# Performance work log

Hardware: AMD Instinct MI355X
Metric: run time of the kernel (lower is better)

The kernel has to match this reference:

```python
import jax, jax.numpy as jnp
import numpy as np

E = 1024   # d_model
H = 16     # nhead
DH = E // H
F = 4096   # dim_feedforward
B, S = 4, 1024
EPS = 1e-5


def setup_inputs() -> dict:
    key = jax.random.key(0)
    ks = jax.random.split(key, 12)
    s = 0.02
    return {
        "src": jax.random.normal(ks[0], (B, S, E), jnp.float32),
        "src_mask": jnp.zeros((S, S), jnp.float32),
        "w_qkv": jax.random.normal(ks[1], (3 * E, E), jnp.float32) * s,
        "b_qkv": jnp.zeros((3 * E,), jnp.float32),
        "w_o": jax.random.normal(ks[2], (E, E), jnp.float32) * s,
        "b_o": jnp.zeros((E,), jnp.float32),
        "w1": jax.random.normal(ks[3], (F, E), jnp.float32) * s,
        "b1": jnp.zeros((F,), jnp.float32),
        "w2": jax.random.normal(ks[4], (E, F), jnp.float32) * s,
        "b2": jnp.zeros((E,), jnp.float32),
        "ln1_g": jnp.ones((E,), jnp.float32),
        "ln1_b": jnp.zeros((E,), jnp.float32),
        "ln2_g": jnp.ones((E,), jnp.float32),
        "ln2_b": jnp.zeros((E,), jnp.float32),
    }


def _layer_norm(x, g, b):
    mu = jnp.mean(x, axis=-1, keepdims=True)
    var = jnp.mean(jnp.square(x - mu), axis=-1, keepdims=True)
    return (x - mu) * jax.lax.rsqrt(var + EPS) * g + b


def reference(src, src_mask, w_qkv, b_qkv, w_o, b_o, w1, b1, w2, b2,
              ln1_g, ln1_b, ln2_g, ln2_b):
    # dropout in eval mode (identity). Math matches nn.MultiheadAttention
    # with need_weights=True, average_attn_weights=False.
    b, s, e = src.shape
    qkv = src @ w_qkv.T + b_qkv                      # [B,S,3E]
    q, k, v = jnp.split(qkv, 3, axis=-1)
    q = q.reshape(b, s, H, DH)
    k = k.reshape(b, s, H, DH)
    v = v.reshape(b, s, H, DH)
    scale = 1.0 / np.sqrt(DH)
    scores = jnp.einsum('bqhd,bkhd->bhqk', q, k) * scale + src_mask  # [B,H,S,S]
    attn_weights = jax.nn.softmax(scores, axis=-1)                   # [B,H,S,S]
    ctx = jnp.einsum('bhqk,bkhd->bqhd', attn_weights, v).reshape(b, s, e)
    attn_out = ctx @ w_o.T + b_o
    x = _layer_norm(src + attn_out, ln1_g, ln1_b)
    ffn = jax.nn.relu(x @ w1.T + b1) @ w2.T + b2
    x = _layer_norm(x + ffn, ln2_g, ln2_b)
    return x, attn_weights
```

## Files before the change

kernel.cpp:

```cpp
#include <hip/hip_runtime.h>
#include <cstdint>

typedef __bf16 bf16;
typedef bf16 bf16x8 __attribute__((ext_vector_type(8)));
typedef bf16 bf16x4 __attribute__((ext_vector_type(4)));
typedef float f32x4 __attribute__((ext_vector_type(4)));
typedef uint32_t u32;

static constexpr int E_ = 1024;
static constexpr int H_ = 16;
static constexpr int DH_ = 64;
static constexpr int F_ = 4096;
static constexpr int B_ = 4;
static constexpr int S_ = 1024;
static constexpr long TOK = (long)B_ * S_;

__device__ static __forceinline__ void gld16(const void* g, void* l) {
  __builtin_amdgcn_global_load_lds(
      (const __attribute__((address_space(1))) u32*)g,
      (__attribute__((address_space(3))) u32*)l, 16, 0, 0);
}

__device__ __forceinline__ f32x4 mfma16(bf16x8 a, bf16x8 b, f32x4 c) {
  return __builtin_amdgcn_mfma_f32_16x16x32_bf16(a, b, c, 0, 0, 0);
}

__global__ __launch_bounds__(256) void f2b_all(
    const float* __restrict__ s0, bf16* __restrict__ d0,
    const float* __restrict__ s1, bf16* __restrict__ d1,
    const float* __restrict__ s2, bf16* __restrict__ d2,
    const float* __restrict__ s3, bf16* __restrict__ d3,
    const float* __restrict__ s4, bf16* __restrict__ d4) {
  long v = (long)blockIdx.x * 256 + threadIdx.x;
  const float* in;
  bf16* out;
  long off;
  if (v < 524288)        { in = s0; out = d0; off = v; }
  else if (v < 917504)   { in = s1; out = d1; off = v - 524288; }
  else if (v < 1048576)  { in = s2; out = d2; off = v - 917504; }
  else if (v < 1572864)  { in = s3; out = d3; off = v - 1048576; }
  else                   { in = s4; out = d4; off = v - 1572864; }
  const float4* p = (const float4*)in + off * 2;
  float4 a = p[0], b = p[1];
  bf16x8 o = {(bf16)a.x, (bf16)a.y, (bf16)a.z, (bf16)a.w,
              (bf16)b.x, (bf16)b.y, (bf16)b.z, (bf16)b.w};
  *((bf16x8*)out + off) = o;
}

enum { G_RELU_BF16 = 0, G_QKV = 1 };

template <int EPI>
__global__ __launch_bounds__(512, 2) void gemm256(
    const bf16* __restrict__ A, const bf16* __restrict__ Bm,
    bf16* __restrict__ Cb, bf16* __restrict__ Qh, bf16* __restrict__ Kh,
    bf16* __restrict__ Vt, const float* __restrict__ bias, int K, int ldc) {
  __shared__ bf16 S[65536];
  bf16* A0 = S;
  bf16* A1 = S + 16384;
  bf16* B0 = S + 32768;
  bf16* B1 = S + 49152;
  const int tid = threadIdx.x, lane = tid & 63, wave = tid >> 6;
  const int quad = lane >> 4, l16 = lane & 15;
  const int wm = wave >> 2, wn = wave & 3;
  const int row0 = blockIdx.y * 256, col0 = blockIdx.x * 256;
  const int NT = K >> 6;

  const long ldab = (long)K * 2;
  const char* Ag = (const char*)A + (long)(row0 + (tid >> 3)) * ldab + (tid & 7) * 16;
  const char* Bg = (const char*)Bm + (long)(col0 + (tid >> 3)) * ldab + (tid & 7) * 16;
  char* A0c = (char*)A0 + tid * 16;
  char* A1c = (char*)A1 + tid * 16;
  char* B0c = (char*)B0 + tid * 16;
  char* B1c = (char*)B1 + tid * 16;

  f32x4 acc[8][4];
#pragma unroll
  for (int m = 0; m < 8; m++)
#pragma unroll
    for (int n = 0; n < 4; n++) acc[m][n] = (f32x4){0.f, 0.f, 0.f, 0.f};

#pragma unroll
  for (int c = 0; c < 4; c++) gld16(Ag + (long)c * 64 * ldab, A0c + c * 8192);
#pragma unroll
  for (int c = 0; c < 4; c++) gld16(Bg + (long)c * 64 * ldab, B0c + c * 8192);
#pragma unroll
  for (int c = 0; c < 4; c++) gld16(Ag + (long)c * 64 * ldab + 128, A1c + c * 8192);

  auto tile = [&](int kt, const bf16* Ac, const bf16* Bc, char* AcS, char* BoS,
                  bool last) {
    if (last)
      asm volatile("s_waitcnt vmcnt(0)" ::: "memory");
    else
      asm volatile("s_waitcnt vmcnt(4)" ::: "memory");
    __builtin_amdgcn_s_barrier();
    if (kt + 1 < NT) {
#pragma unroll
      for (int c = 0; c < 4; c++)
        gld16(Bg + (long)c * 64 * ldab + (long)(kt + 1) * 128, BoS + c * 8192);
    }
    bf16x8 af[8][2], bfr[2];
#pragma unroll
    for (int m = 0; m < 8; m++)
#pragma unroll
      for (int kk = 0; kk < 2; kk++)
        af[m][kk] = *(const bf16x8*)&Ac[(wm * 128 + m * 16 + l16) * 64 + kk * 32 + quad * 8];
#pragma unroll
    for (int kk = 0; kk < 2; kk++)
      bfr[kk] = *(const bf16x8*)&Bc[(wn * 64 + l16) * 64 + kk * 32 + quad * 8];
    __builtin_amdgcn_s_setprio(1);
#pragma unroll
    for (int m = 0; m < 8; m++)
#pragma unroll
      for (int kk = 0; kk < 2; kk++)
        acc[m][0] = mfma16(af[m][kk], bfr[kk], acc[m][0]);
    __builtin_amdgcn_s_setprio(0);
    asm volatile("s_waitcnt lgkmcnt(0)" ::: "memory");
    __builtin_amdgcn_s_barrier();
#pragma unroll
    for (int n = 1; n < 4; n++) {
      if (n < 3 && kt + 2 < NT) {
#pragma unroll
        for (int c = 0; c < 2; c++) {
          int sw = (n - 1) * 2 + c;
          gld16(Ag + (long)sw * 64 * ldab + (long)(kt + 2) * 128, AcS + sw * 8192);
        }
      }
#pragma unroll
      for (int kk = 0; kk < 2; kk++)
        bfr[kk] = *(const bf16x8*)&Bc[(wn * 64 + n * 16 + l16) * 64 + kk * 32 + quad * 8];
      __builtin_amdgcn_s_setprio(1);
#pragma unroll
      for (int m = 0; m < 8; m++)
#pragma unroll
        for (int kk = 0; kk < 2; kk++)
          acc[m][n] = mfma16(af[m][kk], bfr[kk], acc[m][n]);
      __builtin_amdgcn_s_setprio(0);
    }
  };

  for (int kt = 0; kt < NT; kt += 2) {
    tile(kt, A0, B0, A0c, B1c, false);
    tile(kt + 1, A1, B1, A1c, B0c, kt + 2 == NT);
  }

  if constexpr (EPI == G_RELU_BF16) {
#pragma unroll
    for (int m = 0; m < 8; m++)
#pragma unroll
      for (int n = 0; n < 4; n++)
#pragma unroll
        for (int r = 0; r < 4; r++) {
          int row = row0 + wm * 128 + m * 16 + quad * 4 + r;
          int col = col0 + wn * 64 + n * 16 + l16;
          float v = acc[m][n][r] + bias[col];
          Cb[(long)row * ldc + col] = (bf16)fmaxf(v, 0.f);
        }
  } else {
    const int which = col0 >> 10;
    if (which == 2) {
      asm volatile("s_waitcnt lgkmcnt(0) vmcnt(0)" ::: "memory");
      __builtin_amdgcn_s_barrier();
      bf16* T = S;
#pragma unroll
      for (int m = 0; m < 8; m++)
#pragma unroll
        for (int n = 0; n < 4; n++)
#pragma unroll
          for (int r = 0; r < 4; r++) {
            int row_l = wm * 128 + m * 16 + quad * 4 + r;
            int col_l = wn * 64 + n * 16 + l16;
            float t = acc[m][n][r] + bias[col0 + col_l];
            T[col_l * 256 + (row_l ^ ((col_l & 7) << 4))] = (bf16)t;
          }
      __syncthreads();
      const int b_ = row0 >> 10;
      const int s0 = row0 & 1023;
#pragma unroll
      for (int g = 0; g < 8; g++) {
        int col_l = wave * 32 + g * 4 + quad;
        int nn = (col0 + col_l) & 1023;
        int h_ = nn >> 6, d_ = nn & 63;
#pragma unroll
        for (int half = 0; half < 2; half++) {
          int sl = l16 * 8 + half * 128;
          bf16x8 vv = *(const bf16x8*)&T[col_l * 256 + (sl ^ ((col_l & 7) << 4))];
          *(bf16x8*)&Vt[(((long)(b_ * H_ + h_)) * DH_ + d_) * S_ + s0 + sl] = vv;
        }
      }
    } else {
#pragma unroll
      for (int m = 0; m < 8; m++)
#pragma unroll
        for (int n = 0; n < 4; n++)
#pragma unroll
          for (int r = 0; r < 4; r++) {
            int row = row0 + wm * 128 + m * 16 + quad * 4 + r;
            int col = col0 + wn * 64 + n * 16 + l16;
            float t = acc[m][n][r] + bias[col];
            int b_ = row >> 10, s_ = row & 1023;
            int nn = col & 1023;
            int h_ = nn >> 6, d_ = nn & 63;
            long q = (((long)(b_ * H_ + h_)) * S_ + s_) * DH_ + d_;
            if (which == 0) Qh[q] = (bf16)t;
            else Kh[q] = (bf16)t;
          }
    }
  }
}

enum { EPI_BIAS_RES_F32 = 3 };

template <int EPI, int BN>
__global__ __launch_bounds__(256, 2) void gemm_nt(
    const bf16* __restrict__ A, const bf16* __restrict__ Bm,
    float* __restrict__ Cf, bf16* __restrict__ Cb,
    const float* __restrict__ bias, const float* __restrict__ res,
    int K, int ldc) {
  constexpr int NJ = BN / 32;
  __shared__ bf16 Sm[128 * 64 + BN * 64];
  bf16* As = Sm;
  bf16* Bs = Sm + 128 * 64;
  const int tid = threadIdx.x, lane = tid & 63, wave = tid >> 6;
  const int quad = lane >> 4, l16 = lane & 15;
  const int wm = wave >> 1, wn = wave & 1;
  const int row0 = blockIdx.y * 128, col0 = blockIdx.x * BN;

  const long ldab = (long)K * 2;
  const char* Ag = (const char*)A +
                   (long)(row0 + wave * 32 + (lane >> 3)) * ldab + (lane & 7) * 16;
  const char* Bg = (const char*)Bm +
                   (long)(col0 + wave * (BN / 4) + (lane >> 3)) * ldab + (lane & 7) * 16;
  char* Al = (char*)As + (wave * 32 + (lane >> 3)) * 128 + (lane & 7) * 16;
  char* Bl = (char*)Bs + (wave * (BN / 4) + (lane >> 3)) * 128 + (lane & 7) * 16;

  f32x4 acc[4][NJ];
#pragma unroll
  for (int i = 0; i < 4; i++)
#pragma unroll
    for (int j = 0; j < NJ; j++) acc[i][j] = (f32x4){0.f, 0.f, 0.f, 0.f};

  for (int k0 = 0; k0 < K; k0 += 64) {
    __syncthreads();
#pragma unroll
    for (int c = 0; c < 4; c++) gld16(Ag + (long)c * 8 * ldab + k0 * 2, Al + c * 1024);
#pragma unroll
    for (int c = 0; c < BN / 32; c++) gld16(Bg + (long)c * 8 * ldab + k0 * 2, Bl + c * 1024);
    __syncthreads();
#pragma unroll
    for (int kk = 0; kk < 2; kk++) {
      bf16x8 af[4], bfr[NJ];
#pragma unroll
      for (int i = 0; i < 4; i++)
        af[i] = *(const bf16x8*)&As[(wm * 64 + i * 16 + l16) * 64 + kk * 32 + quad * 8];
#pragma unroll
      for (int j = 0; j < NJ; j++)
        bfr[j] = *(const bf16x8*)&Bs[(wn * (BN / 2) + j * 16 + l16) * 64 + kk * 32 + quad * 8];
#pragma unroll
      for (int i = 0; i < 4; i++)
#pragma unroll
        for (int j = 0; j < NJ; j++) acc[i][j] = mfma16(af[i], bfr[j], acc[i][j]);
    }
  }

#pragma unroll
  for (int i = 0; i < 4; i++)
#pragma unroll
    for (int j = 0; j < NJ; j++)
#pragma unroll
      for (int r = 0; r < 4; r++) {
        int row = row0 + wm * 64 + i * 16 + quad * 4 + r;
        int col = col0 + wn * (BN / 2) + j * 16 + l16;
        float v = acc[i][j][r];
        if constexpr (EPI == EPI_BIAS_RES_F32) {
          Cf[(long)row * ldc + col] = v + bias[col] + res[(long)row * ldc + col];
        } else {
          Cb[(long)row * ldc + col] = (bf16)fmaxf(v + bias[col], 0.f);
        }
      }
}

__global__ __launch_bounds__(256, 2) void attn_pass1(
    const bf16* __restrict__ Q, const bf16* __restrict__ K,
    const float* __restrict__ mask, float* __restrict__ rowsum) {
  __shared__ bf16 Qs[128 * 64];
  __shared__ bf16 Ks[128 * 64];
  const int tid = threadIdx.x, lane = tid & 63, wave = tid >> 6;
  const int quad = lane >> 4, l16 = lane & 15;
  const int q0 = blockIdx.x * 128, bh = blockIdx.y;
  const bf16* Qb = Q + ((long)bh * S_ + q0) * DH_;
  const bf16* Kb = K + (long)bh * S_ * DH_;

  {
    const char* g = (const char*)Qb + wave * 4096 + lane * 16;
    char* l = (char*)Qs + wave * 4096 + lane * 16;
#pragma unroll
    for (int c = 0; c < 4; c++) gld16(g + c * 1024, l + c * 1024);
  }

  float rs[2][4];
#pragma unroll
  for (int i = 0; i < 2; i++)
#pragma unroll
    for (int r = 0; r < 4; r++) rs[i][r] = 0.f;

  for (int t = 0; t < 8; t++) {
    __syncthreads();
    {
      const char* g = (const char*)Kb + (long)t * 16384 + wave * 4096 + lane * 16;
      char* l = (char*)Ks + wave * 4096 + lane * 16;
#pragma unroll
      for (int c = 0; c < 4; c++) gld16(g + c * 1024, l + c * 1024);
    }
    __syncthreads();
    f32x4 acc[2][8];
#pragma unroll
    for (int i = 0; i < 2; i++)
#pragma unroll
      for (int j = 0; j < 8; j++) acc[i][j] = (f32x4){0.f, 0.f, 0.f, 0.f};
#pragma unroll
    for (int kk = 0; kk < 2; kk++) {
      bf16x8 af[2], bfr[8];
#pragma unroll
      for (int i = 0; i < 2; i++)
        af[i] = *(const bf16x8*)&Qs[(wave * 32 + i * 16 + l16) * 64 + kk * 32 + quad * 8];
#pragma unroll
      for (int j = 0; j < 8; j++)
        bfr[j] = *(const bf16x8*)&Ks[(j * 16 + l16) * 64 + kk * 32 + quad * 8];
#pragma unroll
      for (int i = 0; i < 2; i++)
#pragma unroll
        for (int j = 0; j < 8; j++) acc[i][j] = mfma16(af[i], bfr[j], acc[i][j]);
    }
#pragma unroll
    for (int i = 0; i < 2; i++)
#pragma unroll
      for (int j = 0; j < 8; j++)
#pragma unroll
        for (int r = 0; r < 4; r++) {
          int qr = q0 + wave * 32 + i * 16 + quad * 4 + r;
          int gcol = t * 128 + j * 16 + l16;
          float sv = acc[i][j][r] * 0.125f + mask[(long)qr * S_ + gcol];
          rs[i][r] += __expf(sv);
        }
  }
#pragma unroll
  for (int i = 0; i < 2; i++)
#pragma unroll
    for (int r = 0; r < 4; r++) {
      float v = rs[i][r];
      v += __shfl_xor(v, 1);
      v += __shfl_xor(v, 2);
      v += __shfl_xor(v, 4);
      v += __shfl_xor(v, 8);
      if (l16 == 0)
        rowsum[(long)bh * S_ + q0 + wave * 32 + i * 16 + quad * 4 + r] = v;
    }
}

__global__ __launch_bounds__(256, 2) void attn_pass2(
    const bf16* __restrict__ Q, const bf16* __restrict__ K,
    const bf16* __restrict__ V, const float* __restrict__ mask,
    const float* __restrict__ rowsum, float* __restrict__ W,
    bf16* __restrict__ ctxb) {
  __shared__ bf16 Qs[128 * 64];
  __shared__ bf16 Ks[128 * 64];
  __shared__ bf16 Ps[128 * 136];
  const int tid = threadIdx.x, lane = tid & 63, wave = tid >> 6;
  const int quad = lane >> 4, l16 = lane & 15;
  const int q0 = blockIdx.x * 128, bh = blockIdx.y;
  const bf16* Qb = Q + ((long)bh * S_ + q0) * DH_;
  const bf16* Kb = K + (long)bh * S_ * DH_;
  const bf16* Vb = V + (long)bh * DH_ * S_;

  float rinv[2][4];
#pragma unroll
  for (int i = 0; i < 2; i++)
#pragma unroll
    for (int r = 0; r < 4; r++)
      rinv[i][r] =
          1.0f / rowsum[(long)bh * S_ + q0 + wave * 32 + i * 16 + quad * 4 + r];

  {
    const char* g = (const char*)Qb + wave * 4096 + lane * 16;
    char* l = (char*)Qs + wave * 4096 + lane * 16;
#pragma unroll
    for (int c = 0; c < 4; c++) gld16(g + c * 1024, l + c * 1024);
  }

  f32x4 cacc[2][4];
#pragma unroll
  for (int i = 0; i < 2; i++)
#pragma unroll
    for (int j = 0; j < 4; j++) cacc[i][j] = (f32x4){0.f, 0.f, 0.f, 0.f};

  for (int t = 0; t < 8; t++) {
    __syncthreads();
    {
      const char* g = (const char*)Kb + (long)t * 16384 + wave * 4096 + lane * 16;
      char* l = (char*)Ks + wave * 4096 + lane * 16;
#pragma unroll
      for (int c = 0; c < 4; c++) gld16(g + c * 1024, l + c * 1024);
    }
    __syncthreads();
    f32x4 acc[2][8];
#pragma unroll
    for (int i = 0; i < 2; i++)
#pragma unroll
      for (int j = 0; j < 8; j++) acc[i][j] = (f32x4){0.f, 0.f, 0.f, 0.f};
#pragma unroll
    for (int kk = 0; kk < 2; kk++) {
      bf16x8 af[2], bfr[8];
#pragma unroll
      for (int i = 0; i < 2; i++)
        af[i] = *(const bf16x8*)&Qs[(wave * 32 + i * 16 + l16) * 64 + kk * 32 + quad * 8];
#pragma unroll
      for (int j = 0; j < 8; j++)
        bfr[j] = *(const bf16x8*)&Ks[(j * 16 + l16) * 64 + kk * 32 + quad * 8];
#pragma unroll
      for (int i = 0; i < 2; i++)
#pragma unroll
        for (int j = 0; j < 8; j++) acc[i][j] = mfma16(af[i], bfr[j], acc[i][j]);
    }
#pragma unroll
    for (int i = 0; i < 2; i++)
#pragma unroll
      for (int j = 0; j < 8; j++)
#pragma unroll
        for (int r = 0; r < 4; r++) {
          int ql = wave * 32 + i * 16 + quad * 4 + r;
          int qr = q0 + ql;
          int col = j * 16 + l16, gcol = t * 128 + col;
          float u = __expf(acc[i][j][r] * 0.125f + mask[(long)qr * S_ + gcol]) *
                    rinv[i][r];
          __builtin_nontemporal_store(u, &W[((long)bh * S_ + qr) * S_ + gcol]);
          Ps[ql * 136 + col] = (bf16)u;
        }
    __syncthreads();
#pragma unroll
    for (int kk = 0; kk < 4; kk++) {
      bf16x8 pf[2], vf[4];
#pragma unroll
      for (int i = 0; i < 2; i++)
        pf[i] = *(const bf16x8*)&Ps[(wave * 32 + i * 16 + l16) * 136 + kk * 32 + quad * 8];
#pragma unroll
      for (int j = 0; j < 4; j++)
        vf[j] = *(const bf16x8*)(Vb + (long)(j * 16 + l16) * S_ + t * 128 +
                                 kk * 32 + quad * 8);
#pragma unroll
      for (int i = 0; i < 2; i++)
#pragma unroll
        for (int j = 0; j < 4; j++) cacc[i][j] = mfma16(pf[i], vf[j], cacc[i][j]);
    }
  }
  const int b_ = bh >> 4, h_ = bh & 15;
#pragma unroll
  for (int i = 0; i < 2; i++)
#pragma unroll
    for (int j = 0; j < 4; j++)
#pragma unroll
      for (int r = 0; r < 4; r++) {
        int qr = q0 + wave * 32 + i * 16 + quad * 4 + r;
        ctxb[((long)b_ * S_ + qr) * E_ + h_ * 64 + j * 16 + l16] =
            (bf16)cacc[i][j][r];
      }
}

__global__ __launch_bounds__(256) void ln_kernel(
    const float* __restrict__ a, const float* __restrict__ g,
    const float* __restrict__ beta, float* __restrict__ outf,
    bf16* __restrict__ outb) {
  const int tid = threadIdx.x;
  const int wave = tid >> 6, lane = tid & 63;
  long base = (long)blockIdx.x * E_ + tid * 4;
  float4 x = *(const float4*)(a + base);
  float s = x.x + x.y + x.z + x.w;
  float sq = x.x * x.x + x.y * x.y + x.z * x.z + x.w * x.w;
#pragma unroll
  for (int o = 32; o; o >>= 1) { s += __shfl_xor(s, o); sq += __shfl_xor(sq, o); }
  __shared__ float rs[4], rq[4];
  if (!lane) { rs[wave] = s; rq[wave] = sq; }
  __syncthreads();
  s = rs[0] + rs[1] + rs[2] + rs[3];
  sq = rq[0] + rq[1] + rq[2] + rq[3];
  float mu = s * (1.f / E_);
  float var = sq * (1.f / E_) - mu * mu;
  float rstd = rsqrtf(var + 1e-5f);
  int c = tid * 4;
  float4 gg = *(const float4*)(g + c);
  float4 bb = *(const float4*)(beta + c);
  float o0 = (x.x - mu) * rstd * gg.x + bb.x;
  float o1 = (x.y - mu) * rstd * gg.y + bb.y;
  float o2 = (x.z - mu) * rstd * gg.z + bb.z;
  float o3 = (x.w - mu) * rstd * gg.w + bb.w;
  if (outf) *(float4*)(outf + base) = make_float4(o0, o1, o2, o3);
  if (outb) {
    bf16x4 ob = {(bf16)o0, (bf16)o1, (bf16)o2, (bf16)o3};
    *(bf16x4*)(outb + base) = ob;
  }
}

extern "C" void kernel_launch(void* const* d_in, const int* in_sizes, int n_in,
                              void* d_out, int out_size, void* d_ws, size_t ws_size,
                              hipStream_t stream) {
  const float* src   = (const float*)d_in[0];
  const float* mask  = (const float*)d_in[1];
  const float* w_qkv = (const float*)d_in[2];
  const float* b_qkv = (const float*)d_in[3];
  const float* w_o   = (const float*)d_in[4];
  const float* b_o   = (const float*)d_in[5];
  const float* w1    = (const float*)d_in[6];
  const float* b1    = (const float*)d_in[7];
  const float* w2    = (const float*)d_in[8];
  const float* b2    = (const float*)d_in[9];
  const float* ln1g  = (const float*)d_in[10];
  const float* ln1b  = (const float*)d_in[11];
  const float* ln2g  = (const float*)d_in[12];
  const float* ln2b  = (const float*)d_in[13];

  float* out = (float*)d_out;
  float* attnW = out + TOK * E_;

  char* w = (char*)d_ws;
  auto alloc = [&](size_t bytes) {
    void* p = w;
    w += (bytes + 255) & ~(size_t)255;
    return p;
  };
  bf16* srcb  = (bf16*)alloc(TOK * E_ * 2);
  bf16* wqkvb = (bf16*)alloc((size_t)3 * E_ * E_ * 2);
  bf16* wob   = (bf16*)alloc((size_t)E_ * E_ * 2);
  bf16* w1b   = (bf16*)alloc((size_t)F_ * E_ * 2);
  bf16* w2b   = (bf16*)alloc((size_t)E_ * F_ * 2);
  bf16* Qh    = (bf16*)alloc((size_t)B_ * H_ * S_ * DH_ * 2);
  bf16* Kh    = (bf16*)alloc((size_t)B_ * H_ * S_ * DH_ * 2);
  bf16* Vt    = (bf16*)alloc((size_t)B_ * H_ * DH_ * S_ * 2);
  bf16* ctxb  = (bf16*)alloc(TOK * E_ * 2);
  float* attn_out = (float*)alloc(TOK * E_ * 4);
  float* x1f  = (float*)alloc(TOK * E_ * 4);
  bf16* x1b   = (bf16*)alloc(TOK * E_ * 2);
  bf16* h1b   = (bf16*)alloc(TOK * (size_t)F_ * 2);
  float* ffn2 = (float*)alloc(TOK * E_ * 4);
  float* rowsum = (float*)alloc((size_t)B_ * H_ * S_ * 4);

  f2b_all<<<8192, 256, 0, stream>>>(src, srcb, w_qkv, wqkvb, w_o, wob,
                                    w1, w1b, w2, w2b);

  gemm256<G_QKV><<<dim3(3 * E_ / 256, TOK / 256), 512, 0, stream>>>(
      srcb, wqkvb, nullptr, Qh, Kh, Vt, b_qkv, E_, 0);

  attn_pass1<<<dim3(S_ / 128, B_ * H_), 256, 0, stream>>>(Qh, Kh, mask, rowsum);
  attn_pass2<<<dim3(S_ / 128, B_ * H_), 256, 0, stream>>>(Qh, Kh, Vt, mask,
                                                          rowsum, attnW, ctxb);

  gemm_nt<EPI_BIAS_RES_F32, 64><<<dim3(E_ / 64, TOK / 128), 256, 0, stream>>>(
      ctxb, wob, attn_out, nullptr, b_o, src, E_, E_);

  ln_kernel<<<TOK, 256, 0, stream>>>(attn_out, ln1g, ln1b, x1f, x1b);

  gemm256<G_RELU_BF16><<<dim3(F_ / 256, TOK / 256), 512, 0, stream>>>(
      x1b, w1b, h1b, nullptr, nullptr, nullptr, b1, E_, F_);

  gemm_nt<EPI_BIAS_RES_F32, 64><<<dim3(E_ / 64, TOK / 128), 256, 0, stream>>>(
      h1b, w2b, ffn2, nullptr, b2, x1f, F_, E_);

  ln_kernel<<<TOK, 256, 0, stream>>>(ffn2, ln2g, ln2b, out, nullptr);
}
```

Before: 622.6 us.

## Swizzle LDS tiles and restructure GEMM inner loop into two M-halves

Applies an XOR swizzle to the global-to-LDS load column offsets and to the LDS fragment reads to reduce bank conflicts. It also reorganises the per-tile compute: A fragments are held for only four M-subtiles at a time, with all four B fragments kept, and the M-halves are processed around the mid-tile barrier. Global prefetches are split into smaller groups interleaved between phases. sched_barriers pin the instruction order. The goal is lower register pressure and fewer LDS conflicts, at the cost of keeping more B fragments live and a more rigid schedule.

```diff
diff --git a/kernel.cpp b/kernel.cpp
--- a/kernel.cpp
+++ b/kernel.cpp
@@ -62,12 +62,14 @@
   const int tid = threadIdx.x, lane = tid & 63, wave = tid >> 6;
   const int quad = lane >> 4, l16 = lane & 15;
   const int wm = wave >> 2, wn = wave & 3;
+  const int sx = ((l16 >> 2) & 1) << 4;
   const int row0 = blockIdx.y * 256, col0 = blockIdx.x * 256;
   const int NT = K >> 6;
 
   const long ldab = (long)K * 2;
-  const char* Ag = (const char*)A + (long)(row0 + (tid >> 3)) * ldab + (tid & 7) * 16;
-  const char* Bg = (const char*)Bm + (long)(col0 + (tid >> 3)) * ldab + (tid & 7) * 16;
+  const int cbs = ((tid & 7) * 16) ^ (((tid >> 5) & 1) << 5);
+  const char* Ag = (const char*)A + (long)(row0 + (tid >> 3)) * ldab + cbs;
+  const char* Bg = (const char*)Bm + (long)(col0 + (tid >> 3)) * ldab + cbs;
   char* A0c = (char*)A0 + tid * 16;
   char* A1c = (char*)A1 + tid * 16;
   char* B0c = (char*)B0 + tid * 16;
@@ -92,48 +94,64 @@
       asm volatile("s_waitcnt vmcnt(0)" ::: "memory");
     else
       asm volatile("s_waitcnt vmcnt(4)" ::: "memory");
+    __builtin_amdgcn_sched_barrier(0);
     __builtin_amdgcn_s_barrier();
+    __builtin_amdgcn_sched_barrier(0);
+    bf16x8 af[4][2], bfr[4][2];
     if (kt + 1 < NT) {
-#pragma unroll
-      for (int c = 0; c < 4; c++)
-        gld16(Bg + (long)c * 64 * ldab + (long)(kt + 1) * 128, BoS + c * 8192);
-    }
-    bf16x8 af[8][2], bfr[2];
-#pragma unroll
-    for (int m = 0; m < 8; m++)
+      gld16(Bg + (long)(kt + 1) * 128, BoS);
+      gld16(Bg + (long)64 * ldab + (long)(kt + 1) * 128, BoS + 8192);
+    }
+#pragma unroll
+    for (int mi = 0; mi < 4; mi++)
 #pragma unroll
       for (int kk = 0; kk < 2; kk++)
-        af[m][kk] = *(const bf16x8*)&Ac[(wm * 128 + m * 16 + l16) * 64 + kk * 32 + quad * 8];
-#pragma unroll
-    for (int kk = 0; kk < 2; kk++)
-      bfr[kk] = *(const bf16x8*)&Bc[(wn * 64 + l16) * 64 + kk * 32 + quad * 8];
-    __builtin_amdgcn_s_setprio(1);
-#pragma unroll
-    for (int m = 0; m < 8; m++)
+        af[mi][kk] = *(const bf16x8*)&Ac[(wm * 128 + mi * 16 + l16) * 64 +
+                                         ((kk * 32 + quad * 8) ^ sx)];
+#pragma unroll
+    for (int n = 0; n < 4; n++) {
 #pragma unroll
       for (int kk = 0; kk < 2; kk++)
-        acc[m][0] = mfma16(af[m][kk], bfr[kk], acc[m][0]);
-    __builtin_amdgcn_s_setprio(0);
+        bfr[n][kk] = *(const bf16x8*)&Bc[(wn * 64 + n * 16 + l16) * 64 +
+                                         ((kk * 32 + quad * 8) ^ sx)];
+      __builtin_amdgcn_s_setprio(1);
+#pragma unroll
+      for (int mi = 0; mi < 4; mi++)
+#pragma unroll
+        for (int kk = 0; kk < 2; kk++)
+          acc[mi][n] = mfma16(af[mi][kk], bfr[n][kk], acc[mi][n]);
+      __builtin_amdgcn_s_setprio(0);
+    }
+    if (kt + 1 < NT) {
+      gld16(Bg + (long)2 * 64 * ldab + (long)(kt + 1) * 128, BoS + 16384);
+      gld16(Bg + (long)3 * 64 * ldab + (long)(kt + 1) * 128, BoS + 24576);
+    }
+#pragma unroll
+    for (int mi = 0; mi < 4; mi++)
+#pragma unroll
+      for (int kk = 0; kk < 2; kk++)
+        af[mi][kk] = *(const bf16x8*)&Ac[(wm * 128 + 64 + mi * 16 + l16) * 64 +
+                                         ((kk * 32 + quad * 8) ^ sx)];
     asm volatile("s_waitcnt lgkmcnt(0)" ::: "memory");
+    __builtin_amdgcn_sched_barrier(0);
     __builtin_amdgcn_s_barrier();
-#pragma unroll
-    for (int n = 1; n < 4; n++) {
-      if (n < 3 && kt + 2 < NT) {
-#pragma unroll
-        for (int c = 0; c < 2; c++) {
-          int sw = (n - 1) * 2 + c;
-          gld16(Ag + (long)sw * 64 * ldab + (long)(kt + 2) * 128, AcS + sw * 8192);
-        }
+    __builtin_amdgcn_sched_barrier(0);
+#pragma unroll
+    for (int n = 0; n < 4; n++) {
+      if (n == 1 && kt + 2 < NT) {
+        gld16(Ag + (long)(kt + 2) * 128, AcS);
+        gld16(Ag + (long)64 * ldab + (long)(kt + 2) * 128, AcS + 8192);
       }
-#pragma unroll
-      for (int kk = 0; kk < 2; kk++)
-        bfr[kk] = *(const bf16x8*)&Bc[(wn * 64 + n * 16 + l16) * 64 + kk * 32 + quad * 8];
+      if (n == 2 && kt + 2 < NT) {
+        gld16(Ag + (long)2 * 64 * ldab + (long)(kt + 2) * 128, AcS + 16384);
+        gld16(Ag + (long)3 * 64 * ldab + (long)(kt + 2) * 128, AcS + 24576);
+      }
       __builtin_amdgcn_s_setprio(1);
 #pragma unroll
-      for (int m = 0; m < 8; m++)
+      for (int mi = 0; mi < 4; mi++)
 #pragma unroll
         for (int kk = 0; kk < 2; kk++)
-          acc[m][n] = mfma16(af[m][kk], bfr[kk], acc[m][n]);
+          acc[4 + mi][n] = mfma16(af[mi][kk], bfr[n][kk], acc[4 + mi][n]);
       __builtin_amdgcn_s_setprio(0);
     }
   };
```

New measurement: 600.5 us. -3.6%, faster.
